# Performance work log

Hardware: AMD Instinct MI355X
Metric: run time of the kernel (lower is better)

Reference implementation:

```python
import jax, jax.numpy as jnp
import numpy as np

D_MODEL = 768
NUM_HEADS = 48
HEAD_CH = D_MODEL // NUM_HEADS  # 16
INNER = 3 * D_MODEL
BATCH = 2
SEQLEN = 2048
SKIP = 1.0
EPS = 1e-6


def setup_inputs() -> dict:
    key = jax.random.key(0)
    ks = jax.random.split(key, 9)
    s_in = 1.0 / np.sqrt(D_MODEL)
    s_out = 1.0 / np.sqrt(D_MODEL)
    return {
        "inputs": jax.random.normal(ks[0], (BATCH, SEQLEN, D_MODEL), jnp.float32),
        "w_in": jax.random.normal(ks[1], (INNER, D_MODEL), jnp.float32) * s_in,
        "b_in": jax.random.normal(ks[2], (INNER,), jnp.float32) * 0.01,
        "w_sf": jax.random.normal(ks[3], (INNER, 3), jnp.float32) * 0.3,  # depthwise conv kernel
        "b_sf": jax.random.normal(ks[4], (INNER,), jnp.float32) * 0.01,
        "h": jax.random.normal(ks[5], (NUM_HEADS, SEQLEN), jnp.float32) * 0.02,  # long filter
        "norm_w": jnp.ones((D_MODEL,), jnp.float32),
        "w_out": jax.random.normal(ks[6], (D_MODEL, D_MODEL), jnp.float32) * s_out,
        "b_out": jax.random.normal(ks[7], (D_MODEL,), jnp.float32) * 0.01,
    }


def reference(inputs, w_in, b_in, w_sf, b_sf, h, norm_w, w_out, b_out):
    B, L, D = inputs.shape
    N, HC = NUM_HEADS, HEAD_CH
    # in_proj: [B, L, 3D]
    u = jnp.einsum('bld,ed->ble', inputs, w_in) + b_in
    u = jnp.transpose(u, (0, 2, 1))  # [B, 3D, L]
    # causal depthwise conv1d, kernel 3, left pad 2
    up = jnp.pad(u, ((0, 0), (0, 0), (2, 0)))
    uc = (w_sf[:, 0:1] * up[:, :, 0:L]
          + w_sf[:, 1:2] * up[:, :, 1:L + 1]
          + w_sf[:, 2:3] * up[:, :, 2:L + 2]
          + b_sf[:, None])  # [B, 3D, L]
    uc = uc.reshape(B, N, 3 * HC, L)
    x0 = uc[:, :, 0:HC, :]            # q  [B, N, HC, L]
    x1 = uc[:, :, HC:2 * HC, :]       # k  [B, N, HC, L]
    v = uc[:, :, 2 * HC:3 * HC, :]    # v  [B, N, HC, L]
    # outer product: [B, HC_i, HC_j, N, L]
    kv = jnp.einsum('bnil,bnjl->bijnl', x1, v)
    # FFT long convolution with h [N, L], broadcast over b,i,j
    fft_size = 2 * L
    k_f = jnp.fft.rfft(h, n=fft_size) / fft_size        # [N, L+1]
    u_f = jnp.fft.rfft(kv, n=fft_size, axis=-1)         # [B, HC, HC, N, L+1]
    hkv = jnp.fft.irfft(u_f * k_f, n=fft_size, axis=-1, norm='forward')[..., :L]
    # contract with q: [B, L, N, HC_j]
    qhkv = jnp.einsum('bijnl,bnil->blnj', hkv, x0)
    y = qhkv.reshape(B, L, D)
    # RMSNorm
    ms = jnp.mean(jnp.square(y), axis=-1, keepdims=True)
    y = y * jax.lax.rsqrt(ms + EPS) * norm_w
    # out_proj + skip
    y = jnp.einsum('bld,ed->ble', y, w_out) + b_out
    return y + inputs * SKIP
```

## Files before the change

kernel.cpp:

```cpp
#include <hip/hip_runtime.h>
#include <hip/hip_bf16.h>
#include <stdint.h>

typedef __bf16 bf16;
typedef __bf16 bf16x4 __attribute__((ext_vector_type(4)));
typedef __bf16 bf16x8 __attribute__((ext_vector_type(8)));
typedef float f32x4 __attribute__((ext_vector_type(4)));
typedef float f32x16 __attribute__((ext_vector_type(16)));

#define D_MODEL 768
#define NUM_HEADS 48
#define HEAD_CH 16
#define INNER 2304
#define BATCH 2
#define SEQLEN 2048
#define M_ROWS (BATCH * SEQLEN)
#define EPSF 1e-6f

__device__ inline void gload_lds16(const void* g, void* l) {
  __builtin_amdgcn_global_load_lds((__attribute__((address_space(1))) void*)(g),
                                   (__attribute__((address_space(3))) void*)(l),
                                   16, 0, 0);
}

__global__ __launch_bounds__(256) void cvt_f32_bf16(
    const float* __restrict__ src, bf16* __restrict__ dst, int n4) {
  const int i = blockIdx.x * 256 + threadIdx.x;
  if (i < n4) {
    const float4 v = ((const float4*)src)[i];
    bf16x4 o;
    o[0] = (bf16)v.x; o[1] = (bf16)v.y; o[2] = (bf16)v.z; o[3] = (bf16)v.w;
    ((bf16x4*)dst)[i] = o;
  }
}

template <int NCOLS, bool ADD_SKIP, typename CT>
__global__ __launch_bounds__(256) void gemm_bt(
    const bf16* __restrict__ A, const bf16* __restrict__ W,
    const float* __restrict__ bias, const float* __restrict__ skip,
    CT* __restrict__ C, int K) {
  __shared__ __align__(16) bf16 As[128 * 32];
  __shared__ __align__(16) bf16 Bs[128 * 32];
  const int t = threadIdx.x;
  const int lane = t & 63, w = t >> 6;
  const int wm = (w >> 1) * 64, wn = (w & 1) * 64;
  const int row16 = lane & 15, quad = lane >> 4;
  const int m0 = blockIdx.x * 128, n0 = blockIdx.y * 128;

  f32x4 zero4 = {0.f, 0.f, 0.f, 0.f};
  f32x4 acc[4][4];
#pragma unroll
  for (int mi = 0; mi < 4; ++mi)
#pragma unroll
    for (int ni = 0; ni < 4; ++ni) acc[mi][ni] = zero4;

  const int arow = t >> 2;
  const int acol = (t & 3) * 8;
  const bf16* Ab = A + (size_t)m0 * K;
  const bf16* Wb = W + (size_t)n0 * K;

  for (int kt = 0; kt < K; kt += 32) {
    gload_lds16(Ab + (size_t)arow * K + kt + acol, As + t * 8);
    gload_lds16(Ab + (size_t)(64 + arow) * K + kt + acol, As + 2048 + t * 8);
    gload_lds16(Wb + (size_t)arow * K + kt + acol, Bs + t * 8);
    gload_lds16(Wb + (size_t)(64 + arow) * K + kt + acol, Bs + 2048 + t * 8);
    __syncthreads();

    bf16x8 af[4], wf[4];
#pragma unroll
    for (int mi = 0; mi < 4; ++mi)
      af[mi] = *(const bf16x8*)&As[(wm + mi * 16 + row16) * 32 + quad * 8];
#pragma unroll
    for (int ni = 0; ni < 4; ++ni)
      wf[ni] = *(const bf16x8*)&Bs[(wn + ni * 16 + row16) * 32 + quad * 8];
#pragma unroll
    for (int mi = 0; mi < 4; ++mi)
#pragma unroll
      for (int ni = 0; ni < 4; ++ni)
        acc[mi][ni] = __builtin_amdgcn_mfma_f32_16x16x32_bf16(
            af[mi], wf[ni], acc[mi][ni], 0, 0, 0);
    __syncthreads();
  }

#pragma unroll
  for (int mi = 0; mi < 4; ++mi) {
#pragma unroll
    for (int ni = 0; ni < 4; ++ni) {
      const int col = n0 + wn + ni * 16 + row16;
      const float bv = bias[col];
#pragma unroll
      for (int r = 0; r < 4; ++r) {
        const int row = m0 + wm + mi * 16 + quad * 4 + r;
        float v = acc[mi][ni][r] + bv;
        if (ADD_SKIP) v += skip[(size_t)row * NCOLS + col];
        C[(size_t)row * NCOLS + col] = (CT)v;
      }
    }
  }
}

__global__ __launch_bounds__(256) void conv_kv(
    const bf16* __restrict__ u, const float* __restrict__ w_sf,
    const float* __restrict__ b_sf, bf16* __restrict__ kk,
    bf16* __restrict__ vv) {
  const int nh = blockIdx.x, b = blockIdx.y, lc = blockIdx.z;
  const int l0 = lc * 128;
  __shared__ __align__(8) bf16 ut[130 * 32];
  const int t = threadIdx.x;
  for (int i = t; i < 130 * 8; i += 256) {
    const int lr = i >> 3, qd = i & 7;
    const int l = l0 - 2 + lr;
    uint2 val;
    val.x = 0u; val.y = 0u;
    if (l >= 0)
      val = *(const uint2*)&u[(size_t)(b * SEQLEN + l) * INNER + nh * 48 + 16 + qd * 4];
    *(uint2*)&ut[lr * 32 + qd * 4] = val;
  }
  __syncthreads();
  const size_t bn = (size_t)(b * NUM_HEADS + nh);
  for (int i = t; i < 128 * 16; i += 256) {
    const int c = i & 15, lr = i >> 4;
    const int e = nh * 48 + 16 + c;
    const float val = w_sf[e * 3 + 0] * (float)ut[lr * 32 + c] +
                      w_sf[e * 3 + 1] * (float)ut[(lr + 1) * 32 + c] +
                      w_sf[e * 3 + 2] * (float)ut[(lr + 2) * 32 + c] + b_sf[e];
    kk[(bn * SEQLEN + l0 + lr) * 16 + c] = (bf16)val;
  }
  for (int i = t; i < 128 * 16; i += 256) {
    const int lr = i & 127, c = i >> 7;
    const int e = nh * 48 + 32 + c;
    const float val = w_sf[e * 3 + 0] * (float)ut[lr * 32 + 16 + c] +
                      w_sf[e * 3 + 1] * (float)ut[(lr + 1) * 32 + 16 + c] +
                      w_sf[e * 3 + 2] * (float)ut[(lr + 2) * 32 + 16 + c] + b_sf[e];
    vv[(bn * 16 + c) * SEQLEN + l0 + lr] = (bf16)val;
  }
}

__global__ __launch_bounds__(256) void attn_kernel(
    const bf16* __restrict__ u, const bf16* __restrict__ kk,
    const bf16* __restrict__ vv, const float* __restrict__ w_sf,
    const float* __restrict__ b_sf, const float* __restrict__ hg,
    float* __restrict__ y) {
  const int nh = blockIdx.x, b = blockIdx.y, q32 = blockIdx.z;
  const int l0 = q32 * 32;
  __shared__ __align__(16) float hx[32 + SEQLEN];
  __shared__ __align__(16) bf16 st[4 * 32 * 40];
  const int t = threadIdx.x;
  for (int i = t; i < 32 + SEQLEN; i += 256)
    hx[i] = (i >= 32) ? hg[nh * SEQLEN + i - 32] : 0.f;
  __syncthreads();

  const int w = t >> 6, lane = t & 63;
  const int l31 = lane & 31, hi = lane >> 5;
  const int row16 = lane & 15, quad = lane >> 4;
  const bf16* ub = u + (size_t)b * SEQLEN * INNER;
  const size_t bn = (size_t)(b * NUM_HEADS + nh);
  const bf16* kb = kk + bn * SEQLEN * 16;
  const bf16* vb = vv + bn * 16 * SEQLEN;

  bf16x8 zf;
#pragma unroll
  for (int j = 0; j < 8; ++j) zf[j] = (bf16)0.f;
  const f32x4 zacc4 = {0.f, 0.f, 0.f, 0.f};
  f32x16 zacc16;
#pragma unroll
  for (int j = 0; j < 16; ++j) zacc16[j] = 0.f;

  bf16x8 qf;
  {
    const int cq = nh * 48 + hi * 8;
    const int l = l0 + l31;
    bf16x8 t2 = *(const bf16x8*)&ub[(size_t)l * INNER + cq];
    bf16x8 t1 = (l >= 1) ? *(const bf16x8*)&ub[(size_t)(l - 1) * INNER + cq] : zf;
    bf16x8 t0 = (l >= 2) ? *(const bf16x8*)&ub[(size_t)(l - 2) * INNER + cq] : zf;
#pragma unroll
    for (int j = 0; j < 8; ++j)
      qf[j] = (bf16)(w_sf[(cq + j) * 3 + 0] * (float)t0[j] +
                     w_sf[(cq + j) * 3 + 1] * (float)t1[j] +
                     w_sf[(cq + j) * 3 + 2] * (float)t2[j] + b_sf[cq + j]);
  }

  bf16* sw = &st[w * 32 * 40];
  f32x4 o0 = zacc4, o1 = zacc4;

  int mc = w * 32;
  bf16x8 kf = zf, vf = zf;
  if (mc <= l0) {
    kf = *(const bf16x8*)&kb[(mc + l31) * 16 + hi * 8];
    vf = *(const bf16x8*)&vb[row16 * SEQLEN + mc + quad * 8];
  }
  for (; mc <= l0; mc += 128) {
    const int mn = mc + 128;
    bf16x8 kf2 = zf, vf2 = zf;
    if (mn <= l0) {
      kf2 = *(const bf16x8*)&kb[(mn + l31) * 16 + hi * 8];
      vf2 = *(const bf16x8*)&vb[row16 * SEQLEN + mn + quad * 8];
    }
    f32x16 s = __builtin_amdgcn_mfma_f32_32x32x16_bf16(kf, qf, zacc16, 0, 0, 0);

    const int hb0 = 32 + (l0 - mc) + l31 - 4 * hi;
#pragma unroll
    for (int g = 0; g < 4; ++g) {
      const float* hp = &hx[hb0 - 8 * g - 3];
      bf16x4 pk;
      pk[0] = (bf16)(s[4 * g + 0] * hp[3]);
      pk[1] = (bf16)(s[4 * g + 1] * hp[2]);
      pk[2] = (bf16)(s[4 * g + 2] * hp[1]);
      pk[3] = (bf16)(s[4 * g + 3] * hp[0]);
      *(bf16x4*)&sw[l31 * 40 + 8 * g + 4 * hi] = pk;
    }
    asm volatile("s_waitcnt lgkmcnt(0)" ::: "memory");
    const bf16x8 sf0 = *(const bf16x8*)&sw[row16 * 40 + quad * 8];
    const bf16x8 sf1 = *(const bf16x8*)&sw[(row16 + 16) * 40 + quad * 8];
    o0 = __builtin_amdgcn_mfma_f32_16x16x32_bf16(sf0, vf, o0, 0, 0, 0);
    o1 = __builtin_amdgcn_mfma_f32_16x16x32_bf16(sf1, vf, o1, 0, 0, 0);
    asm volatile("" ::: "memory");
    kf = kf2; vf = vf2;
  }

  float* ob = (float*)&st[w * 32 * 40];
#pragma unroll
  for (int r = 0; r < 4; ++r) {
    ob[(quad * 4 + r) * 16 + row16] = o0[r];
    ob[(quad * 4 + r + 16) * 16 + row16] = o1[r];
  }
  __syncthreads();
  for (int i = t; i < 32 * 16; i += 256) {
    const int l = i >> 4, j = i & 15;
    float sum = 0.f;
#pragma unroll
    for (int ww = 0; ww < 4; ++ww)
      sum += ((const float*)&st[ww * 32 * 40])[l * 16 + j];
    y[((size_t)(b * SEQLEN + l0 + l) * NUM_HEADS + nh) * 16 + j] = sum;
  }
}

__global__ __launch_bounds__(256) void rmsnorm_k(
    const float* __restrict__ y, const float* __restrict__ nw,
    bf16* __restrict__ yn) {
  const int row = blockIdx.x;
  const int t = threadIdx.x;
  const float* yr = y + (size_t)row * D_MODEL;
  const float v0 = yr[t];
  const float v1 = yr[t + 256];
  const float v2 = yr[t + 512];
  float ss = v0 * v0 + v1 * v1 + v2 * v2;
#pragma unroll
  for (int off = 32; off >= 1; off >>= 1) ss += __shfl_down(ss, off, 64);
  __shared__ float red[4];
  if ((t & 63) == 0) red[t >> 6] = ss;
  __syncthreads();
  const float tot = red[0] + red[1] + red[2] + red[3];
  const float r = rsqrtf(tot * (1.f / 768.f) + EPSF);
  bf16* yo = yn + (size_t)row * D_MODEL;
  yo[t] = (bf16)(v0 * r * nw[t]);
  yo[t + 256] = (bf16)(v1 * r * nw[t + 256]);
  yo[t + 512] = (bf16)(v2 * r * nw[t + 512]);
}

extern "C" void kernel_launch(void* const* d_in, const int* in_sizes, int n_in,
                              void* d_out, int out_size, void* d_ws,
                              size_t ws_size, hipStream_t stream) {
  const float* inputs = (const float*)d_in[0];
  const float* w_in = (const float*)d_in[1];
  const float* b_in = (const float*)d_in[2];
  const float* w_sf = (const float*)d_in[3];
  const float* b_sf = (const float*)d_in[4];
  const float* hb = (const float*)d_in[5];
  const float* norm_w = (const float*)d_in[6];
  const float* w_out = (const float*)d_in[7];
  const float* b_out = (const float*)d_in[8];

  char* ws = (char*)d_ws;
  const size_t U_B = (size_t)M_ROWS * INNER * 2;
  const size_t V_B = (size_t)BATCH * NUM_HEADS * HEAD_CH * SEQLEN * 2;
  const size_t SLOT_B = (size_t)M_ROWS * D_MODEL * 2;
  const size_t WIN_B = (size_t)INNER * D_MODEL * 2;
  bf16* u = (bf16*)(ws);
  bf16* v = (bf16*)(ws + U_B);
  bf16* in16 = (bf16*)(ws + U_B + V_B);
  bf16* k16 = in16;
  bf16* yn = in16;
  bf16* win16 = (bf16*)(ws + U_B + V_B + SLOT_B);
  bf16* wout16 = (bf16*)(ws + U_B + V_B + SLOT_B + WIN_B);
  float* y = (float*)d_out;
  float* out = (float*)d_out;

  const int n4_in = M_ROWS * D_MODEL / 4;
  const int n4_win = INNER * D_MODEL / 4;
  const int n4_wout = D_MODEL * D_MODEL / 4;
  hipLaunchKernelGGL(cvt_f32_bf16, dim3((n4_in + 255) / 256), dim3(256), 0,
                     stream, inputs, in16, n4_in);
  hipLaunchKernelGGL(cvt_f32_bf16, dim3((n4_win + 255) / 256), dim3(256), 0,
                     stream, w_in, win16, n4_win);
  hipLaunchKernelGGL(cvt_f32_bf16, dim3((n4_wout + 255) / 256), dim3(256), 0,
                     stream, w_out, wout16, n4_wout);

  hipLaunchKernelGGL((gemm_bt<INNER, false, bf16>), dim3(32, 18), dim3(256), 0,
                     stream, in16, win16, b_in, (const float*)nullptr, u, 768);
  hipLaunchKernelGGL(conv_kv, dim3(48, 2, 16), dim3(256), 0, stream, u, w_sf,
                     b_sf, k16, v);
  hipLaunchKernelGGL(attn_kernel, dim3(48, 2, 64), dim3(256), 0, stream, u,
                     k16, v, w_sf, b_sf, hb, y);
  hipLaunchKernelGGL(rmsnorm_k, dim3(M_ROWS), dim3(256), 0, stream, y, norm_w,
                     yn);
  hipLaunchKernelGGL((gemm_bt<D_MODEL, true, float>), dim3(32, 6), dim3(256),
                     0, stream, yn, wout16, b_out, inputs, out, 768);
}
```

Measured before the change: 222.1 us.

## Give each wave its own query tile in attention, dropping cross-wave reduction

The attention kernel is re-partitioned. Each block now covers 128 query rows and each wave walks the whole causal key range for its own 32-row tile, where before the key range was split across waves and the partial results were summed through shared memory. Blocks are issued heaviest-first by reversing the tile index. Each block loads only the filter prefix it needs, and the per-wave LDS scratch is double-buffered so the compiler memory fence can go. This removes the block barrier, the LDS reduction and redundant filter loads, at the cost of longer serial MFMA chains per wave and a quarter as many blocks.

```diff
diff --git a/kernel.cpp b/kernel.cpp
--- a/kernel.cpp
+++ b/kernel.cpp
@@ -141,18 +141,21 @@
     const bf16* __restrict__ vv, const float* __restrict__ w_sf,
     const float* __restrict__ b_sf, const float* __restrict__ hg,
     float* __restrict__ y) {
-  const int nh = blockIdx.x, b = blockIdx.y, q32 = blockIdx.z;
-  const int l0 = q32 * 32;
-  __shared__ __align__(16) float hx[32 + SEQLEN];
-  __shared__ __align__(16) bf16 st[4 * 32 * 40];
+  const int zc = (int)gridDim.x - 1 - (int)blockIdx.x;
+  const int nh = blockIdx.y % NUM_HEADS, b = blockIdx.y / NUM_HEADS;
+  const int lbase = zc * 128;
+  __shared__ __align__(16) float hx[2080];
+  __shared__ __align__(16) bf16 st[8 * 32 * 40];
   const int t = threadIdx.x;
-  for (int i = t; i < 32 + SEQLEN; i += 256)
+  const int hlim = 160 + 128 * zc;
+  for (int i = t; i < hlim; i += 256)
     hx[i] = (i >= 32) ? hg[nh * SEQLEN + i - 32] : 0.f;
   __syncthreads();
 
   const int w = t >> 6, lane = t & 63;
   const int l31 = lane & 31, hi = lane >> 5;
   const int row16 = lane & 15, quad = lane >> 4;
+  const int l0w = lbase + 32 * w;
   const bf16* ub = u + (size_t)b * SEQLEN * INNER;
   const size_t bn = (size_t)(b * NUM_HEADS + nh);
   const bf16* kb = kk + bn * SEQLEN * 16;
@@ -169,7 +172,7 @@
   bf16x8 qf;
   {
     const int cq = nh * 48 + hi * 8;
-    const int l = l0 + l31;
+    const int l = l0w + l31;
     bf16x8 t2 = *(const bf16x8*)&ub[(size_t)l * INNER + cq];
     bf16x8 t1 = (l >= 1) ? *(const bf16x8*)&ub[(size_t)(l - 1) * INNER + cq] : zf;
     bf16x8 t0 = (l >= 2) ? *(const bf16x8*)&ub[(size_t)(l - 2) * INNER + cq] : zf;
@@ -180,25 +183,23 @@
                      w_sf[(cq + j) * 3 + 2] * (float)t2[j] + b_sf[cq + j]);
   }
 
-  bf16* sw = &st[w * 32 * 40];
   f32x4 o0 = zacc4, o1 = zacc4;
-
-  int mc = w * 32;
-  bf16x8 kf = zf, vf = zf;
-  if (mc <= l0) {
-    kf = *(const bf16x8*)&kb[(mc + l31) * 16 + hi * 8];
-    vf = *(const bf16x8*)&vb[row16 * SEQLEN + mc + quad * 8];
-  }
-  for (; mc <= l0; mc += 128) {
-    const int mn = mc + 128;
+  const int nsteps = (l0w >> 5) + 1;
+  int sbuf = 0;
+
+  bf16x8 kf = *(const bf16x8*)&kb[l31 * 16 + hi * 8];
+  bf16x8 vf = *(const bf16x8*)&vb[row16 * SEQLEN + quad * 8];
+  for (int s2 = 0; s2 < nsteps; ++s2) {
+    const int mc = s2 * 32;
     bf16x8 kf2 = zf, vf2 = zf;
-    if (mn <= l0) {
-      kf2 = *(const bf16x8*)&kb[(mn + l31) * 16 + hi * 8];
-      vf2 = *(const bf16x8*)&vb[row16 * SEQLEN + mn + quad * 8];
+    if (s2 + 1 < nsteps) {
+      kf2 = *(const bf16x8*)&kb[(mc + 32 + l31) * 16 + hi * 8];
+      vf2 = *(const bf16x8*)&vb[row16 * SEQLEN + mc + 32 + quad * 8];
     }
     f32x16 s = __builtin_amdgcn_mfma_f32_32x32x16_bf16(kf, qf, zacc16, 0, 0, 0);
 
-    const int hb0 = 32 + (l0 - mc) + l31 - 4 * hi;
+    bf16* sw = &st[(w * 2 + sbuf) * 32 * 40];
+    const int hb0 = 32 + (l0w - mc) + l31 - 4 * hi;
 #pragma unroll
     for (int g = 0; g < 4; ++g) {
       const float* hp = &hx[hb0 - 8 * g - 3];
@@ -214,24 +215,14 @@
     const bf16x8 sf1 = *(const bf16x8*)&sw[(row16 + 16) * 40 + quad * 8];
     o0 = __builtin_amdgcn_mfma_f32_16x16x32_bf16(sf0, vf, o0, 0, 0, 0);
     o1 = __builtin_amdgcn_mfma_f32_16x16x32_bf16(sf1, vf, o1, 0, 0, 0);
-    asm volatile("" ::: "memory");
-    kf = kf2; vf = vf2;
-  }
-
-  float* ob = (float*)&st[w * 32 * 40];
+    kf = kf2; vf = vf2; sbuf ^= 1;
+  }
+
 #pragma unroll
   for (int r = 0; r < 4; ++r) {
-    ob[(quad * 4 + r) * 16 + row16] = o0[r];
-    ob[(quad * 4 + r + 16) * 16 + row16] = o1[r];
-  }
-  __syncthreads();
-  for (int i = t; i < 32 * 16; i += 256) {
-    const int l = i >> 4, j = i & 15;
-    float sum = 0.f;
-#pragma unroll
-    for (int ww = 0; ww < 4; ++ww)
-      sum += ((const float*)&st[ww * 32 * 40])[l * 16 + j];
-    y[((size_t)(b * SEQLEN + l0 + l) * NUM_HEADS + nh) * 16 + j] = sum;
+    const int la = l0w + quad * 4 + r;
+    y[((size_t)(b * SEQLEN + la) * NUM_HEADS + nh) * 16 + row16] = o0[r];
+    y[((size_t)(b * SEQLEN + la + 16) * NUM_HEADS + nh) * 16 + row16] = o1[r];
   }
 }
 
@@ -300,8 +291,8 @@
                      stream, in16, win16, b_in, (const float*)nullptr, u, 768);
   hipLaunchKernelGGL(conv_kv, dim3(48, 2, 16), dim3(256), 0, stream, u, w_sf,
                      b_sf, k16, v);
-  hipLaunchKernelGGL(attn_kernel, dim3(48, 2, 64), dim3(256), 0, stream, u,
-                     k16, v, w_sf, b_sf, hb, y);
+  hipLaunchKernelGGL(attn_kernel, dim3(16, 96), dim3(256), 0, stream, u, k16,
+                     v, w_sf, b_sf, hb, y);
   hipLaunchKernelGGL(rmsnorm_k, dim3(M_ROWS), dim3(256), 0, stream, y, norm_w,
                      yn);
   hipLaunchKernelGGL((gemm_bt<D_MODEL, true, float>), dim3(32, 6), dim3(256),
```

Measured after the change: 248.3 us. 1.12x slower.

## Precompute conv q in conv kernel, trim filter staging, reverse attention block order

Applied to the files above, without the earlier changes.

The conv kernel now also produces the convolved q channels into a compact per-head buffer, so the attention kernel no longer recomputes q from the wide u tensor. The attention kernel loads only the filter prefix it needs, masks causality explicitly instead of using a zero-padded filter, and launches the longest query blocks first to reduce tail imbalance. The output projection GEMM uses 64-row tiles to double its grid, and workspace buffers are reshuffled to alias freed regions. This adds an extra q buffer write and read, and relies on correct aliasing of the workspace.

```diff
diff --git a/kernel.cpp b/kernel.cpp
--- a/kernel.cpp
+++ b/kernel.cpp
@@ -34,23 +34,24 @@
   }
 }
 
-template <int NCOLS, bool ADD_SKIP, typename CT>
+template <int TM, int NCOLS, bool ADD_SKIP, typename CT>
 __global__ __launch_bounds__(256) void gemm_bt(
     const bf16* __restrict__ A, const bf16* __restrict__ W,
     const float* __restrict__ bias, const float* __restrict__ skip,
     CT* __restrict__ C, int K) {
-  __shared__ __align__(16) bf16 As[128 * 32];
+  constexpr int MI = TM / 32;
+  __shared__ __align__(16) bf16 As[TM * 32];
   __shared__ __align__(16) bf16 Bs[128 * 32];
   const int t = threadIdx.x;
   const int lane = t & 63, w = t >> 6;
-  const int wm = (w >> 1) * 64, wn = (w & 1) * 64;
+  const int wm = (w >> 1) * (TM / 2), wn = (w & 1) * 64;
   const int row16 = lane & 15, quad = lane >> 4;
-  const int m0 = blockIdx.x * 128, n0 = blockIdx.y * 128;
+  const int m0 = blockIdx.x * TM, n0 = blockIdx.y * 128;
 
   f32x4 zero4 = {0.f, 0.f, 0.f, 0.f};
-  f32x4 acc[4][4];
-#pragma unroll
-  for (int mi = 0; mi < 4; ++mi)
+  f32x4 acc[MI][4];
+#pragma unroll
+  for (int mi = 0; mi < MI; ++mi)
 #pragma unroll
     for (int ni = 0; ni < 4; ++ni) acc[mi][ni] = zero4;
 
@@ -61,20 +62,21 @@
 
   for (int kt = 0; kt < K; kt += 32) {
     gload_lds16(Ab + (size_t)arow * K + kt + acol, As + t * 8);
-    gload_lds16(Ab + (size_t)(64 + arow) * K + kt + acol, As + 2048 + t * 8);
+    if (TM == 128)
+      gload_lds16(Ab + (size_t)(64 + arow) * K + kt + acol, As + 2048 + t * 8);
     gload_lds16(Wb + (size_t)arow * K + kt + acol, Bs + t * 8);
     gload_lds16(Wb + (size_t)(64 + arow) * K + kt + acol, Bs + 2048 + t * 8);
     __syncthreads();
 
-    bf16x8 af[4], wf[4];
-#pragma unroll
-    for (int mi = 0; mi < 4; ++mi)
+    bf16x8 af[MI], wf[4];
+#pragma unroll
+    for (int mi = 0; mi < MI; ++mi)
       af[mi] = *(const bf16x8*)&As[(wm + mi * 16 + row16) * 32 + quad * 8];
 #pragma unroll
     for (int ni = 0; ni < 4; ++ni)
       wf[ni] = *(const bf16x8*)&Bs[(wn + ni * 16 + row16) * 32 + quad * 8];
 #pragma unroll
-    for (int mi = 0; mi < 4; ++mi)
+    for (int mi = 0; mi < MI; ++mi)
 #pragma unroll
       for (int ni = 0; ni < 4; ++ni)
         acc[mi][ni] = __builtin_amdgcn_mfma_f32_16x16x32_bf16(
@@ -83,7 +85,7 @@
   }
 
 #pragma unroll
-  for (int mi = 0; mi < 4; ++mi) {
+  for (int mi = 0; mi < MI; ++mi) {
 #pragma unroll
     for (int ni = 0; ni < 4; ++ni) {
       const int col = n0 + wn + ni * 16 + row16;
@@ -99,62 +101,70 @@
   }
 }
 
-__global__ __launch_bounds__(256) void conv_kv(
+__global__ __launch_bounds__(256) void conv_qkv(
     const bf16* __restrict__ u, const float* __restrict__ w_sf,
-    const float* __restrict__ b_sf, bf16* __restrict__ kk,
-    bf16* __restrict__ vv) {
+    const float* __restrict__ b_sf, bf16* __restrict__ qq,
+    bf16* __restrict__ kk, bf16* __restrict__ vv) {
   const int nh = blockIdx.x, b = blockIdx.y, lc = blockIdx.z;
   const int l0 = lc * 128;
-  __shared__ __align__(8) bf16 ut[130 * 32];
+  __shared__ __align__(8) bf16 ut[130 * 48];
   const int t = threadIdx.x;
-  for (int i = t; i < 130 * 8; i += 256) {
-    const int lr = i >> 3, qd = i & 7;
+  for (int i = t; i < 130 * 12; i += 256) {
+    const int lr = i / 12, qd = i % 12;
     const int l = l0 - 2 + lr;
     uint2 val;
     val.x = 0u; val.y = 0u;
     if (l >= 0)
-      val = *(const uint2*)&u[(size_t)(b * SEQLEN + l) * INNER + nh * 48 + 16 + qd * 4];
-    *(uint2*)&ut[lr * 32 + qd * 4] = val;
+      val = *(const uint2*)&u[(size_t)(b * SEQLEN + l) * INNER + nh * 48 + qd * 4];
+    *(uint2*)&ut[lr * 48 + qd * 4] = val;
   }
   __syncthreads();
   const size_t bn = (size_t)(b * NUM_HEADS + nh);
-  for (int i = t; i < 128 * 16; i += 256) {
-    const int c = i & 15, lr = i >> 4;
-    const int e = nh * 48 + 16 + c;
-    const float val = w_sf[e * 3 + 0] * (float)ut[lr * 32 + c] +
-                      w_sf[e * 3 + 1] * (float)ut[(lr + 1) * 32 + c] +
-                      w_sf[e * 3 + 2] * (float)ut[(lr + 2) * 32 + c] + b_sf[e];
-    kk[(bn * SEQLEN + l0 + lr) * 16 + c] = (bf16)val;
+#pragma unroll
+  for (int s = 0; s < 2; ++s) {
+    bf16* dst = (s == 0) ? qq : kk;
+    const int cb = s * 16;
+    for (int i = t; i < 128 * 16; i += 256) {
+      const int c = i & 15, lr = i >> 4;
+      const int e = nh * 48 + cb + c;
+      const float val = w_sf[e * 3 + 0] * (float)ut[lr * 48 + cb + c] +
+                        w_sf[e * 3 + 1] * (float)ut[(lr + 1) * 48 + cb + c] +
+                        w_sf[e * 3 + 2] * (float)ut[(lr + 2) * 48 + cb + c] +
+                        b_sf[e];
+      dst[(bn * SEQLEN + l0 + lr) * 16 + c] = (bf16)val;
+    }
   }
   for (int i = t; i < 128 * 16; i += 256) {
     const int lr = i & 127, c = i >> 7;
     const int e = nh * 48 + 32 + c;
-    const float val = w_sf[e * 3 + 0] * (float)ut[lr * 32 + 16 + c] +
-                      w_sf[e * 3 + 1] * (float)ut[(lr + 1) * 32 + 16 + c] +
-                      w_sf[e * 3 + 2] * (float)ut[(lr + 2) * 32 + 16 + c] + b_sf[e];
+    const float val = w_sf[e * 3 + 0] * (float)ut[lr * 48 + 32 + c] +
+                      w_sf[e * 3 + 1] * (float)ut[(lr + 1) * 48 + 32 + c] +
+                      w_sf[e * 3 + 2] * (float)ut[(lr + 2) * 48 + 32 + c] +
+                      b_sf[e];
     vv[(bn * 16 + c) * SEQLEN + l0 + lr] = (bf16)val;
   }
 }
 
 __global__ __launch_bounds__(256) void attn_kernel(
-    const bf16* __restrict__ u, const bf16* __restrict__ kk,
-    const bf16* __restrict__ vv, const float* __restrict__ w_sf,
-    const float* __restrict__ b_sf, const float* __restrict__ hg,
+    const bf16* __restrict__ qq, const bf16* __restrict__ kk,
+    const bf16* __restrict__ vv, const float* __restrict__ hg,
     float* __restrict__ y) {
-  const int nh = blockIdx.x, b = blockIdx.y, q32 = blockIdx.z;
+  const int nh = blockIdx.x, b = blockIdx.y;
+  const int q32 = (int)gridDim.z - 1 - (int)blockIdx.z;
   const int l0 = q32 * 32;
-  __shared__ __align__(16) float hx[32 + SEQLEN];
+  __shared__ __align__(16) float hs[SEQLEN];
   __shared__ __align__(16) bf16 st[4 * 32 * 40];
   const int t = threadIdx.x;
-  for (int i = t; i < 32 + SEQLEN; i += 256)
-    hx[i] = (i >= 32) ? hg[nh * SEQLEN + i - 32] : 0.f;
+  const int n4 = (l0 + 32) >> 2;
+  for (int i = t; i < n4; i += 256)
+    ((float4*)hs)[i] = ((const float4*)(hg + nh * SEQLEN))[i];
   __syncthreads();
 
   const int w = t >> 6, lane = t & 63;
   const int l31 = lane & 31, hi = lane >> 5;
   const int row16 = lane & 15, quad = lane >> 4;
-  const bf16* ub = u + (size_t)b * SEQLEN * INNER;
   const size_t bn = (size_t)(b * NUM_HEADS + nh);
+  const bf16* qb = qq + bn * SEQLEN * 16;
   const bf16* kb = kk + bn * SEQLEN * 16;
   const bf16* vb = vv + bn * 16 * SEQLEN;
 
@@ -166,22 +176,10 @@
 #pragma unroll
   for (int j = 0; j < 16; ++j) zacc16[j] = 0.f;
 
-  bf16x8 qf;
-  {
-    const int cq = nh * 48 + hi * 8;
-    const int l = l0 + l31;
-    bf16x8 t2 = *(const bf16x8*)&ub[(size_t)l * INNER + cq];
-    bf16x8 t1 = (l >= 1) ? *(const bf16x8*)&ub[(size_t)(l - 1) * INNER + cq] : zf;
-    bf16x8 t0 = (l >= 2) ? *(const bf16x8*)&ub[(size_t)(l - 2) * INNER + cq] : zf;
-#pragma unroll
-    for (int j = 0; j < 8; ++j)
-      qf[j] = (bf16)(w_sf[(cq + j) * 3 + 0] * (float)t0[j] +
-                     w_sf[(cq + j) * 3 + 1] * (float)t1[j] +
-                     w_sf[(cq + j) * 3 + 2] * (float)t2[j] + b_sf[cq + j]);
-  }
-
+  const bf16x8 qf = *(const bf16x8*)&qb[(l0 + l31) * 16 + hi * 8];
+
+  f32x4 o0 = zacc4, o1 = zacc4;
   bf16* sw = &st[w * 32 * 40];
-  f32x4 o0 = zacc4, o1 = zacc4;
 
   int mc = w * 32;
   bf16x8 kf = zf, vf = zf;
@@ -198,15 +196,18 @@
     }
     f32x16 s = __builtin_amdgcn_mfma_f32_32x32x16_bf16(kf, qf, zacc16, 0, 0, 0);
 
-    const int hb0 = 32 + (l0 - mc) + l31 - 4 * hi;
+    const int hb0 = (l0 - mc) + l31 - 4 * hi;
 #pragma unroll
     for (int g = 0; g < 4; ++g) {
-      const float* hp = &hx[hb0 - 8 * g - 3];
+      const int d3 = hb0 - 8 * g;
       bf16x4 pk;
-      pk[0] = (bf16)(s[4 * g + 0] * hp[3]);
-      pk[1] = (bf16)(s[4 * g + 1] * hp[2]);
-      pk[2] = (bf16)(s[4 * g + 2] * hp[1]);
-      pk[3] = (bf16)(s[4 * g + 3] * hp[0]);
+      {
+        const int m = mc + 8 * g + 4 * hi;
+        pk[0] = (bf16)((m + 0 <= l0 + l31) ? s[4 * g + 0] * hs[d3 - 0] : 0.f);
+        pk[1] = (bf16)((m + 1 <= l0 + l31) ? s[4 * g + 1] * hs[d3 - 1] : 0.f);
+        pk[2] = (bf16)((m + 2 <= l0 + l31) ? s[4 * g + 2] * hs[d3 - 2] : 0.f);
+        pk[3] = (bf16)((m + 3 <= l0 + l31) ? s[4 * g + 3] * hs[d3 - 3] : 0.f);
+      }
       *(bf16x4*)&sw[l31 * 40 + 8 * g + 4 * hi] = pk;
     }
     asm volatile("s_waitcnt lgkmcnt(0)" ::: "memory");
@@ -275,14 +276,14 @@
   const size_t U_B = (size_t)M_ROWS * INNER * 2;
   const size_t V_B = (size_t)BATCH * NUM_HEADS * HEAD_CH * SEQLEN * 2;
   const size_t SLOT_B = (size_t)M_ROWS * D_MODEL * 2;
-  const size_t WIN_B = (size_t)INNER * D_MODEL * 2;
   bf16* u = (bf16*)(ws);
+  bf16* wout16 = (bf16*)(ws);
+  bf16* yn = (bf16*)(ws + (2 << 20));
   bf16* v = (bf16*)(ws + U_B);
   bf16* in16 = (bf16*)(ws + U_B + V_B);
   bf16* k16 = in16;
-  bf16* yn = in16;
   bf16* win16 = (bf16*)(ws + U_B + V_B + SLOT_B);
-  bf16* wout16 = (bf16*)(ws + U_B + V_B + SLOT_B + WIN_B);
+  bf16* q16 = win16;
   float* y = (float*)d_out;
   float* out = (float*)d_out;
 
@@ -293,17 +294,18 @@
                      stream, inputs, in16, n4_in);
   hipLaunchKernelGGL(cvt_f32_bf16, dim3((n4_win + 255) / 256), dim3(256), 0,
                      stream, w_in, win16, n4_win);
+
+  hipLaunchKernelGGL((gemm_bt<128, INNER, false, bf16>), dim3(32, 18),
+                     dim3(256), 0, stream, in16, win16, b_in,
+                     (const float*)nullptr, u, 768);
+  hipLaunchKernelGGL(conv_qkv, dim3(48, 2, 16), dim3(256), 0, stream, u, w_sf,
+                     b_sf, q16, k16, v);
   hipLaunchKernelGGL(cvt_f32_bf16, dim3((n4_wout + 255) / 256), dim3(256), 0,
                      stream, w_out, wout16, n4_wout);
-
-  hipLaunchKernelGGL((gemm_bt<INNER, false, bf16>), dim3(32, 18), dim3(256), 0,
-                     stream, in16, win16, b_in, (const float*)nullptr, u, 768);
-  hipLaunchKernelGGL(conv_kv, dim3(48, 2, 16), dim3(256), 0, stream, u, w_sf,
-                     b_sf, k16, v);
-  hipLaunchKernelGGL(attn_kernel, dim3(48, 2, 64), dim3(256), 0, stream, u,
-                     k16, v, w_sf, b_sf, hb, y);
+  hipLaunchKernelGGL(attn_kernel, dim3(48, 2, 64), dim3(256), 0, stream, q16,
+                     k16, v, hb, y);
   hipLaunchKernelGGL(rmsnorm_k, dim3(M_ROWS), dim3(256), 0, stream, y, norm_w,
                      yn);
-  hipLaunchKernelGGL((gemm_bt<D_MODEL, true, float>), dim3(32, 6), dim3(256),
-                     0, stream, yn, wout16, b_out, inputs, out, 768);
-}
+  hipLaunchKernelGGL((gemm_bt<64, D_MODEL, true, float>), dim3(64, 6),
+                     dim3(256), 0, stream, yn, wout16, b_out, inputs, out, 768);
+}
```

Result: faster. 206.6 us (-7.0%).
